# Kernel optimization log

Measured on AMD Instinct MI355X. Metric: run time of the kernel, lower is better.

The kernel has to match this reference:

```python
import jax, jax.numpy as jnp
import numpy as np

B, C, H, W = 8, 256, 64, 64
CQK = C // 8


def setup_inputs() -> dict:
    key = jax.random.key(0)
    ks = jax.random.split(key, 9)
    s_in = 1.0 / np.sqrt(C)
    return {
        "feature1": jax.random.normal(ks[0], (B, C, H, W), jnp.float32),
        "feature2": jax.random.normal(ks[1], (B, C, H, W), jnp.float32),
        "feature3": jax.random.normal(ks[2], (B, C, H, W), jnp.float32),
        # 1x1 conv weights stored as [out_ch, in_ch]
        "wq": jax.random.uniform(ks[3], (CQK, C), jnp.float32, -s_in, s_in),
        "bq": jax.random.uniform(ks[4], (CQK,), jnp.float32, -s_in, s_in),
        "wk": jax.random.uniform(ks[5], (CQK, C), jnp.float32, -s_in, s_in),
        "bk": jax.random.uniform(ks[6], (CQK,), jnp.float32, -s_in, s_in),
        "wv": jax.random.uniform(ks[7], (C, C), jnp.float32, -s_in, s_in),
        "bv": jax.random.uniform(ks[8], (C,), jnp.float32, -s_in, s_in),
    }


def reference(feature1, feature2, feature3, wq, bq, wk, bk, wv, bv):
    b, c, h, w = feature1.shape
    hw = h * w
    # 1x1 convs == per-pixel channel GEMMs
    q = jnp.einsum('bchw,oc->bohw', feature1, wq) + bq[None, :, None, None]
    k = jnp.einsum('bchw,oc->bohw', feature2, wk) + bk[None, :, None, None]
    v = jnp.einsum('bchw,oc->bohw', feature3, wv) + bv[None, :, None, None]
    q = q.reshape(b, -1, hw).transpose(0, 2, 1)  # [b, hw, cqk]
    k = k.reshape(b, -1, hw)                      # [b, cqk, hw]
    v = v.reshape(b, -1, hw)                      # [b, c, hw]
    attn = jax.nn.softmax(jnp.einsum('bnc,bcm->bnm', q, k), axis=-1)  # [b, hw, hw]
    # fused = value @ attn^T  -> [b, c, hw]
    fused = jnp.einsum('bcm,bnm->bcn', v, attn)
    return fused.reshape(b, c, h, w)
```

## Files before the change

### kernel.cpp

```cpp
#include <hip/hip_runtime.h>
#include <math.h>

#define BATCH 8
#define CH    256
#define HWPIX 4096
#define CQK_  32

typedef __bf16 bf16x8 __attribute__((ext_vector_type(8)));
typedef __bf16 bf16x4 __attribute__((ext_vector_type(4)));
typedef __bf16 bf16x2 __attribute__((ext_vector_type(2)));
typedef float  f32x4  __attribute__((ext_vector_type(4)));

#define FS_STR 68

static __device__ inline bf16x8 ld_frag(const __bf16* p) {
  bf16x4 lo = *(const bf16x4*)p;
  bf16x4 hi = *(const bf16x4*)(p + 4);
  return __builtin_shufflevector(lo, hi, 0, 1, 2, 3, 4, 5, 6, 7);
}

static __device__ inline bf16x8 w_frag(const float* p) {
  const float4 a = *(const float4*)p;
  const float4 b = *(const float4*)(p + 4);
  bf16x8 r;
  r[0] = (__bf16)a.x; r[1] = (__bf16)a.y; r[2] = (__bf16)a.z; r[3] = (__bf16)a.w;
  r[4] = (__bf16)b.x; r[5] = (__bf16)b.y; r[6] = (__bf16)b.z; r[7] = (__bf16)b.w;
  return r;
}

__global__ __launch_bounds__(256, 4) void proj_all(
    const float* __restrict__ f1, const float* __restrict__ f2,
    const float* __restrict__ f3,
    const float* __restrict__ wq, const float* __restrict__ bq,
    const float* __restrict__ wk, const float* __restrict__ bk,
    const float* __restrict__ wv, const float* __restrict__ bv,
    __bf16* __restrict__ qT, __bf16* __restrict__ kT, __bf16* __restrict__ vv)
{
  __shared__ __align__(16) __bf16 f_s[2][64 * FS_STR];
  const int t    = threadIdx.x;
  const int w    = __builtin_amdgcn_readfirstlane(t >> 6);
  const int lane = t & 63;
  const int q16  = lane & 15;
  const int quad = lane >> 4;
  const int b    = blockIdx.z;
  const int n0   = blockIdx.x * 64;
  const int mode = blockIdx.y;

  const int sn  = (t & 15) * 4;
  const int scp = (t >> 4) * 2;
#define STAGE(fb, c0, dst)                                                      \
  {                                                                             \
    _Pragma("unroll") for (int rr = 0; rr < 2; ++rr) {                          \
      const int c = rr * 32 + scp;                                              \
      const float4 a0 = *(const float4*)&(fb)[(size_t)((c0) + c) * HWPIX + sn]; \
      const float4 a1 = *(const float4*)&(fb)[(size_t)((c0) + c + 1) * HWPIX + sn]; \
      _Pragma("unroll") for (int i = 0; i < 4; ++i) {                           \
        bf16x2 pk;                                                              \
        pk[0] = (__bf16)((const float*)&a0)[i];                                 \
        pk[1] = (__bf16)((const float*)&a1)[i];                                 \
        *(bf16x2*)&(dst)[(sn + i) * FS_STR + c] = pk;                           \
      }                                                                         \
    }                                                                           \
  }

  if (mode == 0) {
    const float* f1b = f1 + (size_t)b * CH * HWPIX + n0;
    const float* f2b = f2 + (size_t)b * CH * HWPIX + n0;
    f32x4 accQ[2], accK[2];
#pragma unroll
    for (int i = 0; i < 2; ++i) {
      accQ[i] = (f32x4){0.f, 0.f, 0.f, 0.f};
      accK[i] = (f32x4){0.f, 0.f, 0.f, 0.f};
    }
    for (int c0 = 0; c0 < CH; c0 += 64) {
      STAGE(f1b, c0, f_s[0]);
      STAGE(f2b, c0, f_s[1]);
      __syncthreads();
      bf16x8 afQ[2], afK[2];
#pragma unroll
      for (int kh = 0; kh < 2; ++kh) {
        afQ[kh] = ld_frag(&f_s[0][(16 * w + q16) * FS_STR + 32 * kh + quad * 8]);
        afK[kh] = ld_frag(&f_s[1][(16 * w + q16) * FS_STR + 32 * kh + quad * 8]);
      }
#pragma unroll
      for (int ot = 0; ot < 2; ++ot) {
#pragma unroll
        for (int kh = 0; kh < 2; ++kh) {
          const bf16x8 wfq =
              w_frag(wq + (size_t)(16 * ot + q16) * CH + c0 + 32 * kh + quad * 8);
          accQ[ot] = __builtin_amdgcn_mfma_f32_16x16x32_bf16(afQ[kh], wfq, accQ[ot], 0, 0, 0);
          const bf16x8 wfk =
              w_frag(wk + (size_t)(16 * ot + q16) * CH + c0 + 32 * kh + quad * 8);
          accK[ot] = __builtin_amdgcn_mfma_f32_16x16x32_bf16(afK[kh], wfk, accK[ot], 0, 0, 0);
        }
      }
      __syncthreads();
    }
    const float bq0 = bq[q16], bq1 = bq[16 + q16];
    const float bk0 = bk[q16], bk1 = bk[16 + q16];
#pragma unroll
    for (int r = 0; r < 4; ++r) {
      const size_t row = (size_t)b * HWPIX + n0 + 16 * w + quad * 4 + r;
      qT[row * CQK_ + q16]      = (__bf16)(accQ[0][r] + bq0);
      qT[row * CQK_ + 16 + q16] = (__bf16)(accQ[1][r] + bq1);
      kT[row * CQK_ + q16]      = (__bf16)(accK[0][r] + bk0);
      kT[row * CQK_ + 16 + q16] = (__bf16)(accK[1][r] + bk1);
    }
  } else {
    const int cbase = (mode - 1) * 128;
    const float* f3b = f3 + (size_t)b * CH * HWPIX + n0;
    f32x4 acc[2][4];
#pragma unroll
    for (int ct = 0; ct < 2; ++ct)
#pragma unroll
      for (int nt = 0; nt < 4; ++nt) acc[ct][nt] = (f32x4){0.f, 0.f, 0.f, 0.f};

    for (int c0 = 0; c0 < CH; c0 += 64) {
      STAGE(f3b, c0, f_s[0]);
      __syncthreads();
      bf16x8 af[2][2];
#pragma unroll
      for (int ct = 0; ct < 2; ++ct)
#pragma unroll
        for (int kh = 0; kh < 2; ++kh)
          af[ct][kh] = w_frag(wv + (size_t)(cbase + 64 * ct + 16 * w + q16) * CH
                              + c0 + 32 * kh + quad * 8);
#pragma unroll
      for (int nt = 0; nt < 4; ++nt) {
#pragma unroll
        for (int kh = 0; kh < 2; ++kh) {
          const bf16x8 bfr = ld_frag(&f_s[0][(16 * nt + q16) * FS_STR + 32 * kh + quad * 8]);
#pragma unroll
          for (int ct = 0; ct < 2; ++ct)
            acc[ct][nt] = __builtin_amdgcn_mfma_f32_16x16x32_bf16(
                af[ct][kh], bfr, acc[ct][nt], 0, 0, 0);
        }
      }
      __syncthreads();
    }
#pragma unroll
    for (int ct = 0; ct < 2; ++ct) {
      const float4 bi = *(const float4*)&bv[cbase + 64 * ct + 16 * w + quad * 4];
#pragma unroll
      for (int nt = 0; nt < 4; ++nt) {
#pragma unroll
        for (int r = 0; r < 4; ++r) {
          const int c = cbase + 64 * ct + 16 * w + quad * 4 + r;
          vv[((size_t)b * CH + c) * HWPIX + n0 + 16 * nt + q16] =
              (__bf16)(acc[ct][nt][r] + ((const float*)&bi)[r]);
        }
      }
    }
  }
#undef STAGE
}

__global__ __launch_bounds__(512, 4) void attn_kernel(
    const __bf16* __restrict__ qT, const __bf16* __restrict__ kT,
    const __bf16* __restrict__ vv, float* __restrict__ out)
{
  __shared__ __align__(16) __bf16 p_s[2][64 * 64];
  __shared__ float L_s[2][64];

  const int t    = threadIdx.x;
  const int w    = __builtin_amdgcn_readfirstlane(t >> 6);
  const int lane = t & 63;
  const int q16  = lane & 15;
  const int quad = lane >> 4;
  const int qb   = w & 3;
  const int hb   = w >> 2;
  const int swz  = (q16 & 7) << 4;

  const int b  = blockIdx.x & 7;
  const int q0 = (blockIdx.x >> 3) * 64;

  const __bf16* kTb = kT + (size_t)b * HWPIX * CQK_;
  const size_t koff = (size_t)(32 * hb + q16) * CQK_ + quad * 8;

  const __bf16* vp[2];
#pragma unroll
  for (int ct = 0; ct < 2; ++ct)
    vp[ct] = vv + ((size_t)b * CH + 32 * w + 16 * ct + q16) * HWPIX + quad * 8;

  const bf16x8 qfrag =
      *(const bf16x8*)(qT + ((size_t)b * HWPIX + q0 + 16 * qb + q16) * CQK_ + quad * 8);

  f32x4 oacc[2][4];
#pragma unroll
  for (int i = 0; i < 2; ++i)
#pragma unroll
    for (int j = 0; j < 4; ++j)
      oacc[i][j] = (f32x4){0.f, 0.f, 0.f, 0.f};
  float Lp = 0.f;

  bf16x8 kf[2];
#pragma unroll
  for (int mt = 0; mt < 2; ++mt)
    kf[mt] = *(const bf16x8*)(kTb + koff + mt * 512);
  {
    f32x4 Sv[2];
#pragma unroll
    for (int mt = 0; mt < 2; ++mt)
      Sv[mt] = __builtin_amdgcn_mfma_f32_16x16x32_bf16(
          kf[mt], qfrag, (f32x4){0.f, 0.f, 0.f, 0.f}, 0, 0, 0);
    const __bf16* kb1 = kTb + 64 * CQK_;
#pragma unroll
    for (int mt = 0; mt < 2; ++mt)
      kf[mt] = *(const bf16x8*)(kb1 + koff + mt * 512);
    char* pw = (char*)p_s[0] + (16 * qb + q16) * 128;
#pragma unroll
    for (int mt = 0; mt < 2; ++mt) {
      bf16x4 pk;
#pragma unroll
      for (int r = 0; r < 4; ++r) {
        const float e = __expf(Sv[mt][r]);
        Lp += e;
        pk[r] = (__bf16)e;
      }
      *(bf16x4*)(pw + ((64 * hb + 32 * mt + 8 * quad) ^ swz)) = pk;
    }
  }
  __syncthreads();

  for (int i = 0; i < 64; ++i) {
    bf16x8 vf[2][2];
#pragma unroll
    for (int ct = 0; ct < 2; ++ct)
#pragma unroll
      for (int mh = 0; mh < 2; ++mh)
        vf[ct][mh] = *(const bf16x8*)(vp[ct] + mh * 32);

    const char* pb = (const char*)p_s[i & 1];
    bf16x8 pf[4][2];
#pragma unroll
    for (int nt = 0; nt < 4; ++nt)
#pragma unroll
      for (int mh = 0; mh < 2; ++mh)
        pf[nt][mh] = *(const bf16x8*)(pb + (16 * nt + q16) * 128
                                      + ((64 * mh + 16 * quad) ^ swz));

    if (i < 63) {
      f32x4 Sv[2];
#pragma unroll
      for (int mt = 0; mt < 2; ++mt)
        Sv[mt] = __builtin_amdgcn_mfma_f32_16x16x32_bf16(
            kf[mt], qfrag, (f32x4){0.f, 0.f, 0.f, 0.f}, 0, 0, 0);
      const __bf16* kb2 = kTb + (size_t)((i + 2) & 63) * (64 * CQK_);
#pragma unroll
      for (int mt = 0; mt < 2; ++mt)
        kf[mt] = *(const bf16x8*)(kb2 + koff + mt * 512);
      char* pw = (char*)p_s[(i + 1) & 1] + (16 * qb + q16) * 128;
#pragma unroll
      for (int mt = 0; mt < 2; ++mt) {
        bf16x4 pk;
#pragma unroll
        for (int r = 0; r < 4; ++r) {
          const float e = __expf(Sv[mt][r]);
          Lp += e;
          pk[r] = (__bf16)e;
        }
        *(bf16x4*)(pw + ((64 * hb + 32 * mt + 8 * quad) ^ swz)) = pk;
      }
    }

#pragma unroll
    for (int ct = 0; ct < 2; ++ct)
#pragma unroll
      for (int nt = 0; nt < 4; ++nt)
#pragma unroll
        for (int mh = 0; mh < 2; ++mh)
          oacc[ct][nt] = __builtin_amdgcn_mfma_f32_16x16x32_bf16(
              vf[ct][mh], pf[nt][mh], oacc[ct][nt], 0, 0, 0);

#pragma unroll
    for (int ct = 0; ct < 2; ++ct) vp[ct] += 64;
    __syncthreads();
  }

  Lp += __shfl_xor(Lp, 16);
  Lp += __shfl_xor(Lp, 32);
  if (quad == 0) L_s[hb][16 * qb + q16] = Lp;
  __syncthreads();

  float rinv[4];
#pragma unroll
  for (int nt = 0; nt < 4; ++nt)
    rinv[nt] = 1.0f / (L_s[0][16 * nt + q16] + L_s[1][16 * nt + q16]);

  float* ob = out + ((size_t)b * CH + 32 * w) * HWPIX + q0;
#pragma unroll
  for (int ct = 0; ct < 2; ++ct)
#pragma unroll
    for (int r = 0; r < 4; ++r)
#pragma unroll
      for (int nt = 0; nt < 4; ++nt)
        ob[(size_t)(16 * ct + quad * 4 + r) * HWPIX + 16 * nt + q16] =
            oacc[ct][nt][r] * rinv[nt];
}

extern "C" void kernel_launch(void* const* d_in, const int* in_sizes, int n_in,
                              void* d_out, int out_size, void* d_ws, size_t ws_size,
                              hipStream_t stream)
{
  const float* f1 = (const float*)d_in[0];
  const float* f2 = (const float*)d_in[1];
  const float* f3 = (const float*)d_in[2];
  const float* wq = (const float*)d_in[3];
  const float* bq = (const float*)d_in[4];
  const float* wk = (const float*)d_in[5];
  const float* bk = (const float*)d_in[6];
  const float* wv = (const float*)d_in[7];
  const float* bv = (const float*)d_in[8];
  float* outp = (float*)d_out;

  __bf16* qTw = (__bf16*)d_ws;
  __bf16* kTw = qTw + (size_t)BATCH * HWPIX * CQK_;
  __bf16* vw  = kTw + (size_t)BATCH * HWPIX * CQK_;

  proj_all<<<dim3(64, 3, 8), 256, 0, stream>>>(f1, f2, f3, wq, bq, wk, bk, wv, bv,
                                               qTw, kTw, vw);
  attn_kernel<<<dim3(512), 512, 0, stream>>>(qTw, kTw, vw, outp);
}
```

Measured before the change: 315.2 us.

## Double-buffer V fragments across iterations and use raw barriers with MFMA priority

The V fragment global loads move one iteration ahead using ping-pong register buffers (vfA/vfB), so their latency overlaps the current iteration's MFMAs. The main loop is unrolled by two through a macro. __syncthreads is replaced with an explicit lgkmcnt wait, s_barrier and sched_barrier, which avoids waiting on outstanding global loads at each barrier. The PV MFMA block runs under s_setprio(1). This raises register pressure, and the final iteration issues one redundant wrapped V load.

```diff
diff --git a/kernel.cpp b/kernel.cpp
--- a/kernel.cpp
+++ b/kernel.cpp
@@ -177,10 +177,10 @@
   const __bf16* kTb = kT + (size_t)b * HWPIX * CQK_;
   const size_t koff = (size_t)(32 * hb + q16) * CQK_ + quad * 8;
 
-  const __bf16* vp[2];
+  const __bf16* vbase[2];
 #pragma unroll
   for (int ct = 0; ct < 2; ++ct)
-    vp[ct] = vv + ((size_t)b * CH + 32 * w + 16 * ct + q16) * HWPIX + quad * 8;
+    vbase[ct] = vv + ((size_t)b * CH + 32 * w + 16 * ct + q16) * HWPIX + quad * 8;
 
   const bf16x8 qfrag =
       *(const bf16x8*)(qT + ((size_t)b * HWPIX + q0 + 16 * qb + q16) * CQK_ + quad * 8);
@@ -197,6 +197,14 @@
 #pragma unroll
   for (int mt = 0; mt < 2; ++mt)
     kf[mt] = *(const bf16x8*)(kTb + koff + mt * 512);
+
+  bf16x8 vfA[2][2], vfB[2][2];
+#pragma unroll
+  for (int ct = 0; ct < 2; ++ct)
+#pragma unroll
+    for (int mh = 0; mh < 2; ++mh)
+      vfA[ct][mh] = *(const bf16x8*)(vbase[ct] + mh * 32);
+
   {
     f32x4 Sv[2];
 #pragma unroll
@@ -220,62 +228,70 @@
       *(bf16x4*)(pw + ((64 * hb + 32 * mt + 8 * quad) ^ swz)) = pk;
     }
   }
-  __syncthreads();
-
-  for (int i = 0; i < 64; ++i) {
-    bf16x8 vf[2][2];
-#pragma unroll
-    for (int ct = 0; ct < 2; ++ct)
-#pragma unroll
-      for (int mh = 0; mh < 2; ++mh)
-        vf[ct][mh] = *(const bf16x8*)(vp[ct] + mh * 32);
-
-    const char* pb = (const char*)p_s[i & 1];
-    bf16x8 pf[4][2];
-#pragma unroll
-    for (int nt = 0; nt < 4; ++nt)
-#pragma unroll
-      for (int mh = 0; mh < 2; ++mh)
-        pf[nt][mh] = *(const bf16x8*)(pb + (16 * nt + q16) * 128
-                                      + ((64 * mh + 16 * quad) ^ swz));
-
-    if (i < 63) {
-      f32x4 Sv[2];
-#pragma unroll
-      for (int mt = 0; mt < 2; ++mt)
-        Sv[mt] = __builtin_amdgcn_mfma_f32_16x16x32_bf16(
-            kf[mt], qfrag, (f32x4){0.f, 0.f, 0.f, 0.f}, 0, 0, 0);
-      const __bf16* kb2 = kTb + (size_t)((i + 2) & 63) * (64 * CQK_);
-#pragma unroll
-      for (int mt = 0; mt < 2; ++mt)
-        kf[mt] = *(const bf16x8*)(kb2 + koff + mt * 512);
-      char* pw = (char*)p_s[(i + 1) & 1] + (16 * qb + q16) * 128;
-#pragma unroll
-      for (int mt = 0; mt < 2; ++mt) {
-        bf16x4 pk;
-#pragma unroll
-        for (int r = 0; r < 4; ++r) {
-          const float e = __expf(Sv[mt][r]);
-          Lp += e;
-          pk[r] = (__bf16)e;
-        }
-        *(bf16x4*)(pw + ((64 * hb + 32 * mt + 8 * quad) ^ swz)) = pk;
-      }
-    }
-
-#pragma unroll
-    for (int ct = 0; ct < 2; ++ct)
-#pragma unroll
-      for (int nt = 0; nt < 4; ++nt)
-#pragma unroll
-        for (int mh = 0; mh < 2; ++mh)
-          oacc[ct][nt] = __builtin_amdgcn_mfma_f32_16x16x32_bf16(
-              vf[ct][mh], pf[nt][mh], oacc[ct][nt], 0, 0, 0);
-
-#pragma unroll
-    for (int ct = 0; ct < 2; ++ct) vp[ct] += 64;
-    __syncthreads();
-  }
+  asm volatile("s_waitcnt lgkmcnt(0)" ::: "memory");
+  __builtin_amdgcn_s_barrier();
+  __builtin_amdgcn_sched_barrier(0);
+
+#define ITER(I, VF_CUR, VF_NXT)                                                 \
+  {                                                                             \
+    const int i_ = (I);                                                         \
+                    \
+    const char* pb = (const char*)p_s[i_ & 1];                                  \
+    bf16x8 pf[4][2];                                                            \
+    _Pragma("unroll") for (int nt = 0; nt < 4; ++nt)                            \
+      _Pragma("unroll") for (int mh = 0; mh < 2; ++mh)                          \
+        pf[nt][mh] = *(const bf16x8*)(pb + (16 * nt + q16) * 128                \
+                                      + ((64 * mh + 16 * quad) ^ swz));         \
+                 \
+    {                                                                           \
+      const size_t vt = (size_t)((i_ + 1) & 63) * 64;                           \
+      _Pragma("unroll") for (int ct = 0; ct < 2; ++ct)                          \
+        _Pragma("unroll") for (int mh = 0; mh < 2; ++mh)                        \
+          VF_NXT[ct][mh] = *(const bf16x8*)(vbase[ct] + vt + mh * 32);          \
+    }                                                                           \
+    if (i_ < 63) {                                                              \
+           \
+      f32x4 Sv[2];                                                              \
+      _Pragma("unroll") for (int mt = 0; mt < 2; ++mt)                          \
+        Sv[mt] = __builtin_amdgcn_mfma_f32_16x16x32_bf16(                       \
+            kf[mt], qfrag, (f32x4){0.f, 0.f, 0.f, 0.f}, 0, 0, 0);               \
+                                                  \
+      {                                                                         \
+        const __bf16* kb2 = kTb + (size_t)((i_ + 2) & 63) * (64 * CQK_);        \
+        _Pragma("unroll") for (int mt = 0; mt < 2; ++mt)                        \
+          kf[mt] = *(const bf16x8*)(kb2 + koff + mt * 512);                     \
+      }                                                                         \
+                    \
+      char* pw = (char*)p_s[(i_ + 1) & 1] + (16 * qb + q16) * 128;              \
+      _Pragma("unroll") for (int mt = 0; mt < 2; ++mt) {                        \
+        bf16x4 pk;                                                              \
+        _Pragma("unroll") for (int r = 0; r < 4; ++r) {                         \
+          const float e = __expf(Sv[mt][r]);                                    \
+          Lp += e;                                                              \
+          pk[r] = (__bf16)e;                                                    \
+        }                                                                       \
+        *(bf16x4*)(pw + ((64 * hb + 32 * mt + 8 * quad) ^ swz)) = pk;           \
+      }                                                                         \
+    }                                                                           \
+                                                             \
+    __builtin_amdgcn_s_setprio(1);                                              \
+    _Pragma("unroll") for (int ct = 0; ct < 2; ++ct)                            \
+      _Pragma("unroll") for (int nt = 0; nt < 4; ++nt)                          \
+        _Pragma("unroll") for (int mh = 0; mh < 2; ++mh)                        \
+          oacc[ct][nt] = __builtin_amdgcn_mfma_f32_16x16x32_bf16(               \
+              VF_CUR[ct][mh], pf[nt][mh], oacc[ct][nt], 0, 0, 0);               \
+    __builtin_amdgcn_s_setprio(0);                                              \
+                             \
+    asm volatile("s_waitcnt lgkmcnt(0)" ::: "memory");                          \
+    __builtin_amdgcn_s_barrier();                                               \
+    __builtin_amdgcn_sched_barrier(0);                                          \
+  }
+
+  for (int i = 0; i < 64; i += 2) {
+    ITER(i, vfA, vfB);
+    ITER(i + 1, vfB, vfA);
+  }
+#undef ITER
 
   Lp += __shfl_xor(Lp, 16);
   Lp += __shfl_xor(Lp, 32);
```

New measurement: 332.4 us. 5.4% more time.

## Widen projection blocks to 512 threads and register-prefetch next input chunk

Applied to the files above, without the earlier changes.

The projection kernel now runs 512-thread blocks over a 2-mode grid. In Q/K mode, each half of the block stages and projects one of the two features. In V mode, one block covers all 256 output channels instead of splitting them across two blocks, so f3 is read and staged once per pixel tile rather than twice. The next 64-channel slice of input is loaded into registers while the MFMAs on the current slice run, to overlap global loads with compute. This costs more registers and reduces the block count.

```diff
diff --git a/kernel.cpp b/kernel.cpp
--- a/kernel.cpp
+++ b/kernel.cpp
@@ -28,7 +28,7 @@
   return r;
 }
 
-__global__ __launch_bounds__(256, 4) void proj_all(
+__global__ __launch_bounds__(512, 4) void proj_all(
     const float* __restrict__ f1, const float* __restrict__ f2,
     const float* __restrict__ f3,
     const float* __restrict__ wq, const float* __restrict__ bq,
@@ -46,84 +46,109 @@
   const int n0   = blockIdx.x * 64;
   const int mode = blockIdx.y;
 
-  const int sn  = (t & 15) * 4;
-  const int scp = (t >> 4) * 2;
-#define STAGE(fb, c0, dst)                                                      \
-  {                                                                             \
-    _Pragma("unroll") for (int rr = 0; rr < 2; ++rr) {                          \
-      const int c = rr * 32 + scp;                                              \
-      const float4 a0 = *(const float4*)&(fb)[(size_t)((c0) + c) * HWPIX + sn]; \
-      const float4 a1 = *(const float4*)&(fb)[(size_t)((c0) + c + 1) * HWPIX + sn]; \
-      _Pragma("unroll") for (int i = 0; i < 4; ++i) {                           \
-        bf16x2 pk;                                                              \
-        pk[0] = (__bf16)((const float*)&a0)[i];                                 \
-        pk[1] = (__bf16)((const float*)&a1)[i];                                 \
-        *(bf16x2*)&(dst)[(sn + i) * FS_STR + c] = pk;                           \
-      }                                                                         \
-    }                                                                           \
-  }
-
   if (mode == 0) {
-    const float* f1b = f1 + (size_t)b * CH * HWPIX + n0;
-    const float* f2b = f2 + (size_t)b * CH * HWPIX + n0;
-    f32x4 accQ[2], accK[2];
-#pragma unroll
-    for (int i = 0; i < 2; ++i) {
-      accQ[i] = (f32x4){0.f, 0.f, 0.f, 0.f};
-      accK[i] = (f32x4){0.f, 0.f, 0.f, 0.f};
-    }
+    const int half = t >> 8;
+    const int th   = t & 255;
+    const int sn   = (th & 15) * 4;
+    const int scp  = (th >> 4) * 2;
+    const int qr   = w & 3;
+    const int isK  = w >> 2;
+
+    const float* fsrc = (half ? f2 : f1) + (size_t)b * CH * HWPIX + n0;
+    __bf16* fdst = f_s[half];
+
+    f32x4 acc[2];
+#pragma unroll
+    for (int i = 0; i < 2; ++i) acc[i] = (f32x4){0.f, 0.f, 0.f, 0.f};
+
+    float4 rg[4];
+#pragma unroll
+    for (int rr = 0; rr < 2; ++rr) {
+      const int c = rr * 32 + scp;
+      rg[2 * rr + 0] = *(const float4*)&fsrc[(size_t)(c)     * HWPIX + sn];
+      rg[2 * rr + 1] = *(const float4*)&fsrc[(size_t)(c + 1) * HWPIX + sn];
+    }
+
+    const float* wmat = isK ? wk : wq;
     for (int c0 = 0; c0 < CH; c0 += 64) {
-      STAGE(f1b, c0, f_s[0]);
-      STAGE(f2b, c0, f_s[1]);
       __syncthreads();
-      bf16x8 afQ[2], afK[2];
-#pragma unroll
-      for (int kh = 0; kh < 2; ++kh) {
-        afQ[kh] = ld_frag(&f_s[0][(16 * w + q16) * FS_STR + 32 * kh + quad * 8]);
-        afK[kh] = ld_frag(&f_s[1][(16 * w + q16) * FS_STR + 32 * kh + quad * 8]);
-      }
+#pragma unroll
+      for (int rr = 0; rr < 2; ++rr) {
+        const int c = rr * 32 + scp;
+#pragma unroll
+        for (int i = 0; i < 4; ++i) {
+          bf16x2 pk;
+          pk[0] = (__bf16)((const float*)&rg[2 * rr + 0])[i];
+          pk[1] = (__bf16)((const float*)&rg[2 * rr + 1])[i];
+          *(bf16x2*)&fdst[(sn + i) * FS_STR + c] = pk;
+        }
+      }
+      __syncthreads();
+      if (c0 < CH - 64) {
+#pragma unroll
+        for (int rr = 0; rr < 2; ++rr) {
+          const int c = rr * 32 + scp;
+          rg[2 * rr + 0] = *(const float4*)&fsrc[(size_t)(c0 + 64 + c)     * HWPIX + sn];
+          rg[2 * rr + 1] = *(const float4*)&fsrc[(size_t)(c0 + 64 + c + 1) * HWPIX + sn];
+        }
+      }
+      bf16x8 af[2];
+#pragma unroll
+      for (int kh = 0; kh < 2; ++kh)
+        af[kh] = ld_frag(&f_s[isK][(16 * qr + q16) * FS_STR + 32 * kh + quad * 8]);
 #pragma unroll
       for (int ot = 0; ot < 2; ++ot) {
 #pragma unroll
         for (int kh = 0; kh < 2; ++kh) {
-          const bf16x8 wfq =
-              w_frag(wq + (size_t)(16 * ot + q16) * CH + c0 + 32 * kh + quad * 8);
-          accQ[ot] = __builtin_amdgcn_mfma_f32_16x16x32_bf16(afQ[kh], wfq, accQ[ot], 0, 0, 0);
-          const bf16x8 wfk =
-              w_frag(wk + (size_t)(16 * ot + q16) * CH + c0 + 32 * kh + quad * 8);
-          accK[ot] = __builtin_amdgcn_mfma_f32_16x16x32_bf16(afK[kh], wfk, accK[ot], 0, 0, 0);
-        }
-      }
+          const bf16x8 wf =
+              w_frag(wmat + (size_t)(16 * ot + q16) * CH + c0 + 32 * kh + quad * 8);
+          acc[ot] = __builtin_amdgcn_mfma_f32_16x16x32_bf16(af[kh], wf, acc[ot], 0, 0, 0);
+        }
+      }
+    }
+    const float* bias = isK ? bk : bq;
+    __bf16* outT = isK ? kT : qT;
+    const float b0 = bias[q16], b1 = bias[16 + q16];
+#pragma unroll
+    for (int r = 0; r < 4; ++r) {
+      const size_t row = (size_t)b * HWPIX + n0 + 16 * qr + quad * 4 + r;
+      outT[row * CQK_ + q16]      = (__bf16)(acc[0][r] + b0);
+      outT[row * CQK_ + 16 + q16] = (__bf16)(acc[1][r] + b1);
+    }
+  } else {
+    const int sn = (t & 15) * 4;
+    const int c2 = (t >> 4) * 2;
+    const float* f3b = f3 + (size_t)b * CH * HWPIX + n0;
+
+    f32x4 acc[2][4];
+#pragma unroll
+    for (int ct = 0; ct < 2; ++ct)
+#pragma unroll
+      for (int nt = 0; nt < 4; ++nt) acc[ct][nt] = (f32x4){0.f, 0.f, 0.f, 0.f};
+
+    float4 r0 = *(const float4*)&f3b[(size_t)(c2)     * HWPIX + sn];
+    float4 r1 = *(const float4*)&f3b[(size_t)(c2 + 1) * HWPIX + sn];
+
+    for (int c0 = 0; c0 < CH; c0 += 64) {
       __syncthreads();
-    }
-    const float bq0 = bq[q16], bq1 = bq[16 + q16];
-    const float bk0 = bk[q16], bk1 = bk[16 + q16];
-#pragma unroll
-    for (int r = 0; r < 4; ++r) {
-      const size_t row = (size_t)b * HWPIX + n0 + 16 * w + quad * 4 + r;
-      qT[row * CQK_ + q16]      = (__bf16)(accQ[0][r] + bq0);
-      qT[row * CQK_ + 16 + q16] = (__bf16)(accQ[1][r] + bq1);
-      kT[row * CQK_ + q16]      = (__bf16)(accK[0][r] + bk0);
-      kT[row * CQK_ + 16 + q16] = (__bf16)(accK[1][r] + bk1);
-    }
-  } else {
-    const int cbase = (mode - 1) * 128;
-    const float* f3b = f3 + (size_t)b * CH * HWPIX + n0;
-    f32x4 acc[2][4];
-#pragma unroll
-    for (int ct = 0; ct < 2; ++ct)
-#pragma unroll
-      for (int nt = 0; nt < 4; ++nt) acc[ct][nt] = (f32x4){0.f, 0.f, 0.f, 0.f};
-
-    for (int c0 = 0; c0 < CH; c0 += 64) {
-      STAGE(f3b, c0, f_s[0]);
+#pragma unroll
+      for (int i = 0; i < 4; ++i) {
+        bf16x2 pk;
+        pk[0] = (__bf16)((const float*)&r0)[i];
+        pk[1] = (__bf16)((const float*)&r1)[i];
+        *(bf16x2*)&f_s[0][(sn + i) * FS_STR + c2] = pk;
+      }
       __syncthreads();
+      if (c0 < CH - 64) {
+        r0 = *(const float4*)&f3b[(size_t)(c0 + 64 + c2)     * HWPIX + sn];
+        r1 = *(const float4*)&f3b[(size_t)(c0 + 64 + c2 + 1) * HWPIX + sn];
+      }
       bf16x8 af[2][2];
 #pragma unroll
       for (int ct = 0; ct < 2; ++ct)
 #pragma unroll
         for (int kh = 0; kh < 2; ++kh)
-          af[ct][kh] = w_frag(wv + (size_t)(cbase + 64 * ct + 16 * w + q16) * CH
+          af[ct][kh] = w_frag(wv + (size_t)(32 * w + 16 * ct + q16) * CH
                               + c0 + 32 * kh + quad * 8);
 #pragma unroll
       for (int nt = 0; nt < 4; ++nt) {
@@ -136,23 +161,21 @@
                 af[ct][kh], bfr, acc[ct][nt], 0, 0, 0);
         }
       }
-      __syncthreads();
     }
 #pragma unroll
     for (int ct = 0; ct < 2; ++ct) {
-      const float4 bi = *(const float4*)&bv[cbase + 64 * ct + 16 * w + quad * 4];
+      const float4 bi = *(const float4*)&bv[32 * w + 16 * ct + quad * 4];
 #pragma unroll
       for (int nt = 0; nt < 4; ++nt) {
 #pragma unroll
         for (int r = 0; r < 4; ++r) {
-          const int c = cbase + 64 * ct + 16 * w + quad * 4 + r;
+          const int c = 32 * w + 16 * ct + quad * 4 + r;
           vv[((size_t)b * CH + c) * HWPIX + n0 + 16 * nt + q16] =
               (__bf16)(acc[ct][nt][r] + ((const float*)&bi)[r]);
         }
       }
     }
   }
-#undef STAGE
 }
 
 __global__ __launch_bounds__(512, 4) void attn_kernel(
@@ -317,7 +340,7 @@
   __bf16* kTw = qTw + (size_t)BATCH * HWPIX * CQK_;
   __bf16* vw  = kTw + (size_t)BATCH * HWPIX * CQK_;
 
-  proj_all<<<dim3(64, 3, 8), 256, 0, stream>>>(f1, f2, f3, wq, bq, wk, bk, wv, bv,
+  proj_all<<<dim3(64, 2, 8), 512, 0, stream>>>(f1, f2, f3, wq, bq, wk, bk, wv, bv,
                                                qTw, kTw, vw);
   attn_kernel<<<dim3(512), 512, 0, stream>>>(qTw, kTw, vw, outp);
 }
```

Result: faster. 305.4 us (-3.1%).
